# Kernel tuning notes

Measured on AMD Instinct MI355X. Metric: run time of the kernel, lower is better.

Reference implementation:

```python
import jax, jax.numpy as jnp
import numpy as np

INPUT, HIDDEN, OUTPUT = 512, 1024, 512
B, T = 64, 512


def setup_inputs() -> dict:
    key = jax.random.key(0)
    ks = jax.random.split(key, 10)
    s_ih = (2.0 / (INPUT + HIDDEN)) ** 0.5
    s_hh = (2.0 / (INPUT + HIDDEN)) ** 0.5
    s_hy = (2.0 / (HIDDEN + OUTPUT)) ** 0.5
    inp = {
        "x": jax.random.normal(ks[0], (B, T, INPUT), dtype=jnp.float32),
        "W_xi": jax.random.normal(ks[1], (INPUT, HIDDEN), dtype=jnp.float32) * s_ih,
        "W_hi": jax.random.normal(ks[2], (HIDDEN, HIDDEN), dtype=jnp.float32) * s_hh,
        "b_i": jnp.zeros((HIDDEN,), dtype=jnp.float32),
        "W_xf": jax.random.normal(ks[3], (INPUT, HIDDEN), dtype=jnp.float32) * s_ih,
        "W_hf": jax.random.normal(ks[4], (HIDDEN, HIDDEN), dtype=jnp.float32) * s_hh,
        "b_f": jnp.zeros((HIDDEN,), dtype=jnp.float32),
        "W_xo": jax.random.normal(ks[5], (INPUT, HIDDEN), dtype=jnp.float32) * s_ih,
        "W_ho": jax.random.normal(ks[6], (HIDDEN, HIDDEN), dtype=jnp.float32) * s_hh,
        "b_o": jnp.zeros((HIDDEN,), dtype=jnp.float32),
        "W_xc": jax.random.normal(ks[7], (INPUT, HIDDEN), dtype=jnp.float32) * s_ih,
        "W_hc": jax.random.normal(ks[8], (HIDDEN, HIDDEN), dtype=jnp.float32) * s_hh,
        "b_c": jnp.zeros((HIDDEN,), dtype=jnp.float32),
        "W_hy": jax.random.normal(ks[9], (HIDDEN, OUTPUT), dtype=jnp.float32) * s_hy,
        "b_y": jnp.zeros((OUTPUT,), dtype=jnp.float32),
    }
    return inp


def reference(x, W_xi, W_hi, b_i, W_xf, W_hf, b_f, W_xo, W_ho, b_o,
              W_xc, W_hc, b_c, W_hy, b_y):
    Bn, Tn, _ = x.shape
    H = W_hi.shape[0]
    # Precompute input projections for all timesteps (one big GEMM per gate).
    xi = jnp.einsum('bti,ih->bth', x, W_xi) + b_i  # [B,T,H]
    xf = jnp.einsum('bti,ih->bth', x, W_xf) + b_f
    xo = jnp.einsum('bti,ih->bth', x, W_xo) + b_o
    xc = jnp.einsum('bti,ih->bth', x, W_xc) + b_c
    # time-major for scan
    xs = (jnp.swapaxes(xi, 0, 1), jnp.swapaxes(xf, 0, 1),
          jnp.swapaxes(xo, 0, 1), jnp.swapaxes(xc, 0, 1))

    def step(carry, xt):
        h, c = carry
        xi_t, xf_t, xo_t, xc_t = xt
        i_t = jax.nn.sigmoid(xi_t + h @ W_hi)
        f_t = jax.nn.sigmoid(xf_t + h @ W_hf)
        o_t = jax.nn.sigmoid(xo_t + h @ W_ho)
        cand = jnp.tanh(xc_t + h @ W_hc)
        c = f_t * c + i_t * cand
        h = o_t * jnp.tanh(c)
        return (h, c), h

    h0 = jnp.zeros((Bn, H), dtype=x.dtype)
    c0 = jnp.zeros((Bn, H), dtype=x.dtype)
    _, hs = jax.lax.scan(step, (h0, c0), xs)  # hs: [T,B,H]
    # Output projection applied to every step's hidden state.
    ys = jnp.einsum('tbh,ho->tbo', hs, W_hy) + b_y
    return jnp.swapaxes(ys, 0, 1)  # [B,T,O]
```

## Files before the change

kernel.cpp:

```cpp
#include <hip/hip_runtime.h>
#include <hip/hip_bf16.h>
#include <cstdint>

#define B_   64
#define T_   512
#define IN_  512
#define H_   1024
#define O_   512
#define NG   4096
#define KC   1536
#define BT   32768
#define BH   65536
#define NWG  256

#define GLB __attribute__((address_space(1)))
#define LDSAS __attribute__((address_space(3)))

using bs8 = __attribute__((ext_vector_type(8))) short;
using f4  = __attribute__((ext_vector_type(4))) float;

__device__ __forceinline__ ushort f2bf(float f) {
    union { float f; uint32_t u; } v; v.f = f;
    uint32_t r = v.u + 0x7fffu + ((v.u >> 16) & 1u);
    return (ushort)(r >> 16);
}
__device__ __forceinline__ float sigm(float x) { return 1.f / (1.f + __expf(-x)); }
__device__ __forceinline__ float tanh_(float x) {
    x = fminf(fmaxf(x, -15.f), 15.f);
    float e = __expf(2.f * x);
    return (e - 1.f) / (e + 1.f);
}


__global__ void k_pack_x(const float* __restrict__ x, ushort* __restrict__ xP) {
    const int n8 = BT * IN_ / 8;
    for (int i = blockIdx.x * blockDim.x + threadIdx.x; i < n8; i += gridDim.x * blockDim.x) {
        const int e8 = i & 3, b = (i >> 2) & 63, kk = (i >> 8) & 15, t = i >> 12;
        const float* s = x + ((size_t)b * T_ + t) * IN_ + kk * 32 + e8 * 8;
        f4 v0 = *reinterpret_cast<const f4*>(s);
        f4 v1 = *reinterpret_cast<const f4*>(s + 4);
        uint4 q;
        q.x = (uint32_t)f2bf(v0[0]) | ((uint32_t)f2bf(v0[1]) << 16);
        q.y = (uint32_t)f2bf(v0[2]) | ((uint32_t)f2bf(v0[3]) << 16);
        q.z = (uint32_t)f2bf(v1[0]) | ((uint32_t)f2bf(v1[1]) << 16);
        q.w = (uint32_t)f2bf(v1[2]) | ((uint32_t)f2bf(v1[3]) << 16);
        *reinterpret_cast<uint4*>(xP + ((size_t)t * 16 + kk) * 2048 + b * 32 + e8 * 8) = q;
    }
}

__global__ void k_build_wcT(const float* __restrict__ xi, const float* __restrict__ xf,
                            const float* __restrict__ xo, const float* __restrict__ xc,
                            const float* __restrict__ hi, const float* __restrict__ hf,
                            const float* __restrict__ ho, const float* __restrict__ hc,
                            ushort* __restrict__ dst) {
    const int total = NG * KC;
    for (int i = blockIdx.x * blockDim.x + threadIdx.x; i < total; i += gridDim.x * blockDim.x) {
        int n = i / KC, k = i - n * KC;
        int g = n & 3, h = n >> 2;
        float v;
        if (k < IN_) {
            const float* s = (g == 0) ? xi : ((g == 1) ? xf : ((g == 2) ? xo : xc));
            v = s[(size_t)k * H_ + h];
        } else {
            const float* s = (g == 0) ? hi : ((g == 1) ? hf : ((g == 2) ? ho : hc));
            v = s[(size_t)(k - IN_) * H_ + h];
        }
        dst[i] = f2bf(v);
    }
}

__global__ void k_build_whyT(const float* __restrict__ w, ushort* __restrict__ dst) {
    const int total = O_ * H_;
    for (int i = blockIdx.x * blockDim.x + threadIdx.x; i < total; i += gridDim.x * blockDim.x) {
        int o = i >> 10, k = i & (H_ - 1);
        dst[i] = f2bf(w[(size_t)k * O_ + o]);
    }
}

__global__ void k_build_bias(const float* __restrict__ bi, const float* __restrict__ bff,
                             const float* __restrict__ bo, const float* __restrict__ bc,
                             float* __restrict__ dst) {
    int i = blockIdx.x * blockDim.x + threadIdx.x;
    if (i < NG) {
        int g = i & 3, h = i >> 2;
        dst[i] = (g == 0) ? bi[h] : ((g == 1) ? bff[h] : ((g == 2) ? bo[h] : bc[h]));
    }
}

__global__ void __launch_bounds__(256, 1)
k_persist(const ushort* __restrict__ WcT, const ushort* __restrict__ xP,
          ushort* __restrict__ hs, float* __restrict__ cst,
          const float* __restrict__ biasc, uint32_t* __restrict__ flags,
          int t0, int nsteps) {
    __shared__ ushort Hst[32 * 2048];
    __shared__ ushort hout[64][4];
    const int g = blockIdx.x, tid = threadIdx.x;
    const int lane = tid & 63, w = tid >> 6;
    const int n0 = g * 16;
    const int l15 = lane & 15, lq = lane >> 4;

    bs8 wf[48];
#pragma unroll
    for (int c = 0; c < 48; ++c)
        wf[c] = *reinterpret_cast<const bs8*>(WcT + (size_t)(n0 + l15) * KC + c * 32 + lq * 8);

    const int bmy = w * 16 + l15;
    const int u = g * 4 + lq;
    const f4 bia = *reinterpret_cast<const f4*>(biasc + n0 + lq * 4);
    float creg = (t0 == 0) ? 0.f : cst[(size_t)bmy * H_ + u];

    const ushort* xb = xP + (size_t)bmy * 32 + lq * 8;

    bs8 xv[16];
#pragma unroll
    for (int c = 0; c < 16; ++c)
        xv[c] = *reinterpret_cast<const bs8*>(xb + ((size_t)t0 * 16 + c) * 2048);

    __syncthreads();

    for (int s = 0; s < nsteps; ++s) {
        const ushort* hslot = hs + (size_t)s * BH;
#pragma unroll
        for (int j = 0; j < 8; ++j) {
            const int c = w * 8 + j;
            const ushort* gp = hslot + (size_t)c * 2048 + (size_t)lane * 8;
            ushort* lp = &Hst[c * 2048];
#pragma unroll
            for (int i = 0; i < 4; ++i)
                __builtin_amdgcn_global_load_lds((const GLB uint32_t*)(gp + i * 512),
                                                 (LDSAS uint32_t*)(lp + i * 512), 16, 0, 0);
        }

        f4 a0 = {0.f,0.f,0.f,0.f}, a1 = {0.f,0.f,0.f,0.f};
        f4 a2 = {0.f,0.f,0.f,0.f}, a3 = {0.f,0.f,0.f,0.f};
#pragma unroll
        for (int c = 0; c < 16; c += 4) {
            a0 = __builtin_amdgcn_mfma_f32_16x16x32_bf16(wf[c + 0], xv[c + 0], a0, 0, 0, 0);
            a1 = __builtin_amdgcn_mfma_f32_16x16x32_bf16(wf[c + 1], xv[c + 1], a1, 0, 0, 0);
            a2 = __builtin_amdgcn_mfma_f32_16x16x32_bf16(wf[c + 2], xv[c + 2], a2, 0, 0, 0);
            a3 = __builtin_amdgcn_mfma_f32_16x16x32_bf16(wf[c + 3], xv[c + 3], a3, 0, 0, 0);
        }

        asm volatile("s_waitcnt vmcnt(0)" ::: "memory");
        __syncthreads();

        const char* hstb = (const char*)&Hst[0] + (size_t)bmy * 64 + lq * 16;
#pragma unroll
        for (int c = 0; c < 32; c += 4) {
            bs8 h0 = *reinterpret_cast<const bs8*>(hstb + (size_t)(c + 0) * 4096);
            bs8 h1 = *reinterpret_cast<const bs8*>(hstb + (size_t)(c + 1) * 4096);
            bs8 h2 = *reinterpret_cast<const bs8*>(hstb + (size_t)(c + 2) * 4096);
            bs8 h3 = *reinterpret_cast<const bs8*>(hstb + (size_t)(c + 3) * 4096);
            a0 = __builtin_amdgcn_mfma_f32_16x16x32_bf16(wf[16 + c + 0], h0, a0, 0, 0, 0);
            a1 = __builtin_amdgcn_mfma_f32_16x16x32_bf16(wf[16 + c + 1], h1, a1, 0, 0, 0);
            a2 = __builtin_amdgcn_mfma_f32_16x16x32_bf16(wf[16 + c + 2], h2, a2, 0, 0, 0);
            a3 = __builtin_amdgcn_mfma_f32_16x16x32_bf16(wf[16 + c + 3], h3, a3, 0, 0, 0);
        }
        f4 ssum = (a0 + a1) + (a2 + a3);

        {
            float pi = ssum[0] + bia[0], pf = ssum[1] + bia[1];
            float po = ssum[2] + bia[2], pc = ssum[3] + bia[3];
            float iv = sigm(pi), fv = sigm(pf), ov = sigm(po), cv = tanh_(pc);
            creg = fv * creg + iv * cv;
            hout[bmy][lq] = f2bf(ov * tanh_(creg));
        }
        __syncthreads();

        if (w == 0) {
            uint2 hv2 = *reinterpret_cast<uint2*>(&hout[lane][0]);
            ushort* dst = hs + (size_t)(s + 1) * BH + (size_t)(g >> 3) * 2048
                        + (size_t)lane * 32 + (g & 7) * 4;
            asm volatile("global_store_dwordx2 %0, %1, off sc0 sc1" :: "v"(dst), "v"(hv2) : "memory");
            asm volatile("s_waitcnt vmcnt(0)" ::: "memory");
            if (tid == 0)
                __hip_atomic_store(&flags[g], (uint32_t)(s + 1),
                                   __ATOMIC_RELAXED, __HIP_MEMORY_SCOPE_AGENT);
        }

        if (s + 1 < nsteps) {
#pragma unroll
            for (int c = 0; c < 16; ++c)
                xv[c] = *reinterpret_cast<const bs8*>(xb + ((size_t)(t0 + s + 1) * 16 + c) * 2048);
            if (w == 0) {
                const uint32_t tgt = (uint32_t)(s + 1);
                for (;;) {
                    uint32_t f0 = __hip_atomic_load(&flags[lane],       __ATOMIC_RELAXED, __HIP_MEMORY_SCOPE_AGENT);
                    uint32_t f1 = __hip_atomic_load(&flags[64 + lane],  __ATOMIC_RELAXED, __HIP_MEMORY_SCOPE_AGENT);
                    uint32_t f2 = __hip_atomic_load(&flags[128 + lane], __ATOMIC_RELAXED, __HIP_MEMORY_SCOPE_AGENT);
                    uint32_t f3 = __hip_atomic_load(&flags[192 + lane], __ATOMIC_RELAXED, __HIP_MEMORY_SCOPE_AGENT);
                    if (__all((int)(f0 >= tgt && f1 >= tgt && f2 >= tgt && f3 >= tgt))) break;
                    __builtin_amdgcn_s_sleep(1);
                }
            }
            __syncthreads();
        }
    }

    cst[(size_t)bmy * H_ + u] = creg;
}

__global__ void __launch_bounds__(64) k_yproj(const ushort* __restrict__ WhyT,
                                              const ushort* __restrict__ hsbase,
                                              const float* __restrict__ by,
                                              float* __restrict__ out, int t_off) {
    const int lane = threadIdx.x;
    const int tloc = blockIdx.x;
    const int o0 = blockIdx.y * 64;
    const int l15 = lane & 15, lq = lane >> 4, lk = lq * 8;
    const int t = t_off + tloc;

    const ushort* slot = hsbase + (size_t)(tloc + 1) * BH;
    const ushort* apm[4]; const ushort* bp[4];
#pragma unroll
    for (int m = 0; m < 4; ++m) apm[m] = WhyT + (size_t)(o0 + m * 16 + l15) * H_ + lk;
#pragma unroll
    for (int n = 0; n < 4; ++n) bp[n] = slot + (size_t)(n * 16 + l15) * 32 + lk;

    f4 acc[4][4] = {};
    for (int kk = 0; kk < 32; ++kk) {
        bs8 a[4], b[4];
#pragma unroll
        for (int m = 0; m < 4; ++m) a[m] = *reinterpret_cast<const bs8*>(apm[m] + kk * 32);
#pragma unroll
        for (int n = 0; n < 4; ++n) b[n] = *reinterpret_cast<const bs8*>(bp[n] + (size_t)kk * 2048);
#pragma unroll
        for (int m = 0; m < 4; ++m)
#pragma unroll
            for (int n = 0; n < 4; ++n)
                acc[m][n] = __builtin_amdgcn_mfma_f32_16x16x32_bf16(a[m], b[n], acc[m][n], 0, 0, 0);
    }

#pragma unroll
    for (int m = 0; m < 4; ++m) {
        const int ob = o0 + m * 16 + lq * 4;
        const f4 bb = *reinterpret_cast<const f4*>(by + ob);
#pragma unroll
        for (int n = 0; n < 4; ++n) {
            const int b_ = n * 16 + l15;
            f4 v = acc[m][n] + bb;
            *reinterpret_cast<f4*>(out + ((size_t)b_ * T_ + t) * O_ + ob) = v;
        }
    }
}


extern "C" void kernel_launch(void* const* d_in, const int* in_sizes, int n_in,
                              void* d_out, int out_size, void* d_ws, size_t ws_size,
                              hipStream_t stream) {
    const float* x   = (const float*)d_in[0];
    const float* wxi = (const float*)d_in[1];
    const float* whi = (const float*)d_in[2];
    const float* bi  = (const float*)d_in[3];
    const float* wxf = (const float*)d_in[4];
    const float* whf = (const float*)d_in[5];
    const float* bf_ = (const float*)d_in[6];
    const float* wxo = (const float*)d_in[7];
    const float* who = (const float*)d_in[8];
    const float* bo  = (const float*)d_in[9];
    const float* wxc = (const float*)d_in[10];
    const float* whc = (const float*)d_in[11];
    const float* bc  = (const float*)d_in[12];
    const float* why = (const float*)d_in[13];
    const float* by  = (const float*)d_in[14];
    float* out = (float*)d_out;

    uint8_t* w = (uint8_t*)d_ws;
    ushort*   xP    = (ushort*)  (w);
    ushort*   WcT   = (ushort*)  (w + 33554432);
    ushort*   WhyT  = (ushort*)  (w + 46137344);
    float*    biasc = (float*)   (w + 47185920);
    float*    cst   = (float*)   (w + 47202304);
    uint32_t* flags = (uint32_t*)(w + 47464448);
    ushort*   hs    = (ushort*)  (w + 47468544);
    const size_t NEED_A = 47468544 + (size_t)(T_ + 1) * BH * 2;
    const size_t NEED_B = 47468544 + (size_t)65 * BH * 2;
    if (ws_size < NEED_B) return;
    const bool fullhs = (ws_size >= NEED_A);

    k_pack_x<<<2048, 256, 0, stream>>>(x, xP);
    k_build_wcT<<<4096, 256, 0, stream>>>(wxi, wxf, wxo, wxc, whi, whf, who, whc, WcT);
    k_build_whyT<<<512, 256, 0, stream>>>(why, WhyT);
    k_build_bias<<<16, 256, 0, stream>>>(bi, bf_, bo, bc, biasc);

    hipMemsetAsync(cst, 0, (size_t)BH * 4, stream);
    hipMemsetAsync(hs,  0, (size_t)BH * 2, stream);

    const int nchunk = fullhs ? 1 : 8;
    const int steps  = fullhs ? T_ : 64;
    for (int c = 0; c < nchunk; ++c) {
        const int t0 = c * steps;
        hipMemsetAsync(flags, 0, NWG * 4, stream);
        const ushort* a0 = WcT; const ushort* a1 = xP; ushort* a2 = hs;
        float* a3 = cst; const float* a4 = biasc; uint32_t* a5 = flags;
        int a6 = t0, a7 = steps;
        void* args[8] = {&a0, &a1, &a2, &a3, &a4, &a5, &a6, &a7};
        hipError_t e = hipLaunchCooperativeKernel((const void*)k_persist,
                                                  dim3(NWG), dim3(256), args, 0, stream);
        if (e != hipSuccess) {
            k_persist<<<dim3(NWG), dim3(256), 0, stream>>>(WcT, xP, hs, cst, biasc,
                                                           flags, t0, steps);
        }
        if (!fullhs) {
            k_yproj<<<dim3(64, O_ / 64), 64, 0, stream>>>(WhyT, hs, by, out, t0);
            if (c != nchunk - 1)
                hipMemcpyAsync(hs, hs + (size_t)64 * BH, (size_t)BH * 2,
                               hipMemcpyDeviceToDevice, stream);
        }
    }
    if (fullhs)
        k_yproj<<<dim3(T_, O_ / 64), 64, 0, stream>>>(WhyT, hs, by, out, 0);
}
```

Before: 3.288 ms.

## Re-layout hidden-state slots and pipeline per-wave h loads with MFMA consumption

Changes the global layout of the hidden-state buffer so each workgroup writes its 4-column block contiguously. Each wave now loads only its own batch rows into a private LDS region, removing the block-wide barrier before the recurrent GEMM. The recurrent MFMAs are consumed in four chunks gated by partial vmcnt waits, so later loads overlap earlier compute. The flag poll becomes a single dwordx4 load per lane, and the output projection is adapted to read the new hs layout with 8-byte loads, which may cost some bandwidth there.

```diff
diff --git a/kernel.cpp b/kernel.cpp
--- a/kernel.cpp
+++ b/kernel.cpp
@@ -18,6 +18,7 @@
 
 using bs8 = __attribute__((ext_vector_type(8))) short;
 using f4  = __attribute__((ext_vector_type(4))) float;
+using u32x4 = __attribute__((ext_vector_type(4))) unsigned int;
 
 __device__ __forceinline__ ushort f2bf(float f) {
     union { float f; uint32_t u; } v; v.f = f;
@@ -87,12 +88,12 @@
     }
 }
 
-__global__ void __launch_bounds__(256, 1)
+__global__ void __launch_bounds__(256) __attribute__((amdgpu_waves_per_eu(1, 1)))
 k_persist(const ushort* __restrict__ WcT, const ushort* __restrict__ xP,
           ushort* __restrict__ hs, float* __restrict__ cst,
           const float* __restrict__ biasc, uint32_t* __restrict__ flags,
           int t0, int nsteps) {
-    __shared__ ushort Hst[32 * 2048];
+    __shared__ char Hst[4][32][1024];
     __shared__ ushort hout[64][4];
     const int g = blockIdx.x, tid = threadIdx.x;
     const int lane = tid & 63, w = tid >> 6;
@@ -109,7 +110,10 @@
     const f4 bia = *reinterpret_cast<const f4*>(biasc + n0 + lq * 4);
     float creg = (t0 == 0) ? 0.f : cst[(size_t)bmy * H_ + u];
 
+    const int lgo = ((lane >> 3) * 512) + (w * 128) + ((lane & 7) * 16);
+    const char* hsb = (const char*)hs;
     const ushort* xb = xP + (size_t)bmy * 32 + lq * 8;
+    const int lro = ((l15 >> 1) * 16) + ((l15 & 1) * 8);
 
     bs8 xv[16];
 #pragma unroll
@@ -118,45 +122,46 @@
 
     __syncthreads();
 
+    f4 acc[4];
+    auto hcons = [&](int c) {
+        const char* base = &Hst[w][c][0] + lro;
+        union { bs8 v; uint2 p[2]; } uu;
+        uu.p[0] = *reinterpret_cast<const uint2*>(base + (lq * 2 + 0) * 128);
+        uu.p[1] = *reinterpret_cast<const uint2*>(base + (lq * 2 + 1) * 128);
+        acc[c & 3] = __builtin_amdgcn_mfma_f32_16x16x32_bf16(wf[16 + c], uu.v, acc[c & 3], 0, 0, 0);
+    };
+
     for (int s = 0; s < nsteps; ++s) {
-        const ushort* hslot = hs + (size_t)s * BH;
-#pragma unroll
-        for (int j = 0; j < 8; ++j) {
-            const int c = w * 8 + j;
-            const ushort* gp = hslot + (size_t)c * 2048 + (size_t)lane * 8;
-            ushort* lp = &Hst[c * 2048];
-#pragma unroll
-            for (int i = 0; i < 4; ++i)
-                __builtin_amdgcn_global_load_lds((const GLB uint32_t*)(gp + i * 512),
-                                                 (LDSAS uint32_t*)(lp + i * 512), 16, 0, 0);
-        }
-
-        f4 a0 = {0.f,0.f,0.f,0.f}, a1 = {0.f,0.f,0.f,0.f};
-        f4 a2 = {0.f,0.f,0.f,0.f}, a3 = {0.f,0.f,0.f,0.f};
-#pragma unroll
-        for (int c = 0; c < 16; c += 4) {
-            a0 = __builtin_amdgcn_mfma_f32_16x16x32_bf16(wf[c + 0], xv[c + 0], a0, 0, 0, 0);
-            a1 = __builtin_amdgcn_mfma_f32_16x16x32_bf16(wf[c + 1], xv[c + 1], a1, 0, 0, 0);
-            a2 = __builtin_amdgcn_mfma_f32_16x16x32_bf16(wf[c + 2], xv[c + 2], a2, 0, 0, 0);
-            a3 = __builtin_amdgcn_mfma_f32_16x16x32_bf16(wf[c + 3], xv[c + 3], a3, 0, 0, 0);
-        }
-
+        const char* slot = hsb + (size_t)s * 131072 + lgo;
+#pragma unroll
+        for (int c = 0; c < 32; ++c)
+            __builtin_amdgcn_global_load_lds((const GLB uint32_t*)(slot + c * 4096),
+                                             (LDSAS uint32_t*)(&Hst[w][c][0]), 16, 0, 0);
+
+#pragma unroll
+        for (int c = 0; c < 4; ++c) acc[c] = (f4){0.f, 0.f, 0.f, 0.f};
+#pragma unroll
+        for (int c = 0; c < 16; ++c)
+            acc[c & 3] = __builtin_amdgcn_mfma_f32_16x16x32_bf16(wf[c], xv[c], acc[c & 3], 0, 0, 0);
+
+        asm volatile("s_waitcnt vmcnt(24)" ::: "memory");
+        __builtin_amdgcn_sched_barrier(0);
+#pragma unroll
+        for (int j = 0; j < 8; ++j) hcons(j);
+        asm volatile("s_waitcnt vmcnt(16)" ::: "memory");
+        __builtin_amdgcn_sched_barrier(0);
+#pragma unroll
+        for (int j = 8; j < 16; ++j) hcons(j);
+        asm volatile("s_waitcnt vmcnt(8)" ::: "memory");
+        __builtin_amdgcn_sched_barrier(0);
+#pragma unroll
+        for (int j = 16; j < 24; ++j) hcons(j);
         asm volatile("s_waitcnt vmcnt(0)" ::: "memory");
-        __syncthreads();
-
-        const char* hstb = (const char*)&Hst[0] + (size_t)bmy * 64 + lq * 16;
-#pragma unroll
-        for (int c = 0; c < 32; c += 4) {
-            bs8 h0 = *reinterpret_cast<const bs8*>(hstb + (size_t)(c + 0) * 4096);
-            bs8 h1 = *reinterpret_cast<const bs8*>(hstb + (size_t)(c + 1) * 4096);
-            bs8 h2 = *reinterpret_cast<const bs8*>(hstb + (size_t)(c + 2) * 4096);
-            bs8 h3 = *reinterpret_cast<const bs8*>(hstb + (size_t)(c + 3) * 4096);
-            a0 = __builtin_amdgcn_mfma_f32_16x16x32_bf16(wf[16 + c + 0], h0, a0, 0, 0, 0);
-            a1 = __builtin_amdgcn_mfma_f32_16x16x32_bf16(wf[16 + c + 1], h1, a1, 0, 0, 0);
-            a2 = __builtin_amdgcn_mfma_f32_16x16x32_bf16(wf[16 + c + 2], h2, a2, 0, 0, 0);
-            a3 = __builtin_amdgcn_mfma_f32_16x16x32_bf16(wf[16 + c + 3], h3, a3, 0, 0, 0);
-        }
-        f4 ssum = (a0 + a1) + (a2 + a3);
+        __builtin_amdgcn_sched_barrier(0);
+#pragma unroll
+        for (int j = 24; j < 32; ++j) hcons(j);
+
+        f4 ssum = (acc[0] + acc[1]) + (acc[2] + acc[3]);
 
         {
             float pi = ssum[0] + bia[0], pf = ssum[1] + bia[1];
@@ -169,8 +174,7 @@
 
         if (w == 0) {
             uint2 hv2 = *reinterpret_cast<uint2*>(&hout[lane][0]);
-            ushort* dst = hs + (size_t)(s + 1) * BH + (size_t)(g >> 3) * 2048
-                        + (size_t)lane * 32 + (g & 7) * 4;
+            char* dst = (char*)hs + (size_t)(s + 1) * 131072 + (size_t)g * 512 + lane * 8;
             asm volatile("global_store_dwordx2 %0, %1, off sc0 sc1" :: "v"(dst), "v"(hv2) : "memory");
             asm volatile("s_waitcnt vmcnt(0)" ::: "memory");
             if (tid == 0)
@@ -184,12 +188,13 @@
                 xv[c] = *reinterpret_cast<const bs8*>(xb + ((size_t)(t0 + s + 1) * 16 + c) * 2048);
             if (w == 0) {
                 const uint32_t tgt = (uint32_t)(s + 1);
+                const uint32_t* fp = flags + lane * 4;
                 for (;;) {
-                    uint32_t f0 = __hip_atomic_load(&flags[lane],       __ATOMIC_RELAXED, __HIP_MEMORY_SCOPE_AGENT);
-                    uint32_t f1 = __hip_atomic_load(&flags[64 + lane],  __ATOMIC_RELAXED, __HIP_MEMORY_SCOPE_AGENT);
-                    uint32_t f2 = __hip_atomic_load(&flags[128 + lane], __ATOMIC_RELAXED, __HIP_MEMORY_SCOPE_AGENT);
-                    uint32_t f3 = __hip_atomic_load(&flags[192 + lane], __ATOMIC_RELAXED, __HIP_MEMORY_SCOPE_AGENT);
-                    if (__all((int)(f0 >= tgt && f1 >= tgt && f2 >= tgt && f3 >= tgt))) break;
+                    u32x4 f;
+                    asm volatile("global_load_dwordx4 %0, %1, off sc0 sc1\n\t"
+                                 "s_waitcnt vmcnt(0)"
+                                 : "=v"(f) : "v"(fp) : "memory");
+                    if (__all((int)(f.x >= tgt && f.y >= tgt && f.z >= tgt && f.w >= tgt))) break;
                     __builtin_amdgcn_s_sleep(1);
                 }
             }
@@ -210,12 +215,10 @@
     const int l15 = lane & 15, lq = lane >> 4, lk = lq * 8;
     const int t = t_off + tloc;
 
-    const ushort* slot = hsbase + (size_t)(tloc + 1) * BH;
-    const ushort* apm[4]; const ushort* bp[4];
+    const char* slot = (const char*)(hsbase + (size_t)(tloc + 1) * BH);
+    const ushort* apm[4];
 #pragma unroll
     for (int m = 0; m < 4; ++m) apm[m] = WhyT + (size_t)(o0 + m * 16 + l15) * H_ + lk;
-#pragma unroll
-    for (int n = 0; n < 4; ++n) bp[n] = slot + (size_t)(n * 16 + l15) * 32 + lk;
 
     f4 acc[4][4] = {};
     for (int kk = 0; kk < 32; ++kk) {
@@ -223,7 +226,13 @@
 #pragma unroll
         for (int m = 0; m < 4; ++m) a[m] = *reinterpret_cast<const bs8*>(apm[m] + kk * 32);
 #pragma unroll
-        for (int n = 0; n < 4; ++n) b[n] = *reinterpret_cast<const bs8*>(bp[n] + (size_t)kk * 2048);
+        for (int n = 0; n < 4; ++n) {
+            const int bb = n * 16 + l15;
+            union { bs8 v; uint2 p[2]; } uu;
+            uu.p[0] = *reinterpret_cast<const uint2*>(slot + (size_t)(kk * 8 + lq * 2 + 0) * 512 + bb * 8);
+            uu.p[1] = *reinterpret_cast<const uint2*>(slot + (size_t)(kk * 8 + lq * 2 + 1) * 512 + bb * 8);
+            b[n] = uu.v;
+        }
 #pragma unroll
         for (int m = 0; m < 4; ++m)
 #pragma unroll
```

Result: faster. 2.695 ms (-18.1%).
